# Performance work log

Measured on AMD Instinct MI355X. Metric: run time of the kernel, lower is better.

Reference implementation:

```python
import jax, jax.numpy as jnp
import numpy as np

IN_FEATURES = 4096
OUT_FEATURES = 11008
BLOCK_SIZE = 64

NF4_TABLE = jnp.array([-1.0, -0.6961928009986877, -0.5250730514526367, -0.39491748809814453,
                       -0.28444138169288635, -0.18477343022823334, -0.09105003625154495, 0.0,
                       0.07958029955625534, 0.16093020141124725, 0.24611230194568634,
                       0.33791524171829224, 0.44070982933044434, 0.5626170039176941,
                       0.7229568362236023, 1.0], dtype=jnp.float32)


def setup_inputs() -> dict:
    key = jax.random.key(0)
    k1, k2, k3, k4 = jax.random.split(key, 4)
    n = IN_FEATURES * OUT_FEATURES
    x = jax.random.normal(k1, (4, 128, IN_FEATURES), dtype=jnp.float32)
    # packed 4-bit codes: two codes per byte, flat layout as produced by quantize_and_pack_nf4
    packed_kernel = jax.random.randint(k2, (n // 2,), 0, 256, dtype=jnp.int32).astype(jnp.uint8)
    # per-block absmax scales (positive)
    scales = jax.random.uniform(k3, (n // BLOCK_SIZE,), minval=0.01, maxval=0.05, dtype=jnp.float32)
    bias = jax.random.normal(k4, (OUT_FEATURES,), dtype=jnp.float32) * 0.01
    return {"x": x, "packed_kernel": packed_kernel, "scales": scales, "bias": bias}


def _dequantize_nf4(packed, absmax, block_size):
    high = (packed >> 4) & 15
    low = packed & 15
    # interleave: [h0, l0, h1, l1, ...] matching jnp.stack([high, low], axis=1).reshape(-1)
    unpacked = jnp.stack([high, low], axis=1).reshape(-1)
    deq = NF4_TABLE[unpacked]                       # [n] fp32
    deq = deq.reshape(-1, block_size) * absmax[:, None]  # per-block scaling
    return deq


def reference(x, packed_kernel, scales, bias):
    kernel = _dequantize_nf4(packed_kernel, scales, BLOCK_SIZE).reshape(IN_FEATURES, OUT_FEATURES)
    y = jnp.einsum("bsi,io->bso", x, kernel)
    y = y + bias
    return y
```

## Files before the change

kernel.cpp:

```cpp
#include <hip/hip_runtime.h>
#include <hip/hip_bf16.h>
#include <hip/hip_fp16.h>
#include <stdint.h>

#define K_DIM 4096
#define N_DIM 11008
#define M_DIM 512
#define PK_ROW 5504
#define SC_ROW 172

typedef __attribute__((ext_vector_type(4))) float f32x4;
typedef __attribute__((ext_vector_type(4))) int i32x4;
typedef __attribute__((ext_vector_type(4))) unsigned int u32x4;
typedef __attribute__((ext_vector_type(8))) _Float16 half8;
typedef __attribute__((ext_vector_type(8))) short bf16x8;

__constant__ float NF4[16] = {
    -1.0f, -0.6961928009986877f, -0.5250730514526367f, -0.39491748809814453f,
    -0.28444138169288635f, -0.18477343022823334f, -0.09105003625154495f, 0.0f,
    0.07958029955625534f, 0.16093020141124725f, 0.24611230194568634f,
    0.33791524171829224f, 0.44070982933044434f, 0.5626170039176941f,
    0.7229568362236023f, 1.0f};

union H8 { u32x4 v; half8 h; };

__device__ __forceinline__ unsigned h2mul(unsigned a, unsigned b) {
  union { __half2 h; unsigned u; } x, y, r;
  x.u = a; y.u = b;
  r.h = x.h * y.h;
  return r.u;
}
__device__ __forceinline__ unsigned hpack(float a, float b) {
  union { __half2 h; unsigned u; } c;
  c.h = __floats2half2_rn(a, b);
  return c.u;
}
__device__ __forceinline__ unsigned f2bf(float v) {
  union { __hip_bfloat16 h; unsigned short u; } cv;
  cv.h = __float2bfloat16(v);
  return (unsigned)cv.u;
}

__global__ __launch_bounds__(256) void prep_all(
    const float* __restrict__ x, const int* __restrict__ packed,
    const float* __restrict__ scales, unsigned* __restrict__ wsa,
    unsigned* __restrict__ codes, unsigned* __restrict__ scalesp) {
  const int bid = blockIdx.x;
  const int t = threadIdx.x;
  if (bid < 5504) {
    const int kt = bid & 63;
    const int nt = bid >> 6;
    __shared__ unsigned char Sb[128 * 36];
    const int npl = t & 63;
    const int kq = t >> 6;
    const int np = nt * 64 + npl;
#pragma unroll
    for (int i = 0; i < 8; ++i) {
      const int kpl = kq + i * 4;
      const int k = kt * 64 + kpl * 2;
      const int w0 = packed[(size_t)k * PK_ROW + np];
      const int w1 = packed[(size_t)(k + 1) * PK_ROW + np];
      Sb[(npl * 2) * 36 + kpl] =
          (unsigned char)((((w0 >> 4) & 15) << 4) | ((w1 >> 4) & 15));
      Sb[(npl * 2 + 1) * 36 + kpl] =
          (unsigned char)(((w0 & 15) << 4) | (w1 & 15));
    }
    __syncthreads();
#pragma unroll
    for (int i = 0; i < 4; ++i) {
      const int lin = t + 256 * i;
      const int n16 = lin & 15;
      const int kp4l = (lin >> 4) & 7;
      const int nb16l = lin >> 7;
      const unsigned v = *(const unsigned*)(Sb + (nb16l * 16 + n16) * 36 + kp4l * 4);
      const size_t D = ((size_t)(nt * 8 + nb16l) * 512 + kt * 8 + kp4l) * 16 + n16;
      codes[D] = v;
    }
  } else if (bid < 6528) {
    const int wid = (bid - 5504) * 4 + (t >> 6);
    const int lane = t & 63;
    const int m16 = wid >> 7, k32 = wid & 127;
    const int m = m16 * 16 + (lane & 15);
    const int k = k32 * 32 + (lane >> 4) * 8;
    const float* src = x + (size_t)m * K_DIM + k;
    f32x4 v0 = *(const f32x4*)src;
    f32x4 v1 = *(const f32x4*)(src + 4);
    u32x4 d;
    d[0] = hpack(v0[0], v0[1]);
    d[1] = hpack(v0[2], v0[3]);
    d[2] = hpack(v1[0], v1[1]);
    d[3] = hpack(v1[2], v1[3]);
    *(u32x4*)(wsa + (size_t)wid * 256 + lane * 4) = d;
  } else {
    const int g = (bid - 6528) * 256 + t;
    if (g < SC_ROW * 2048) {
      const int kp = g / SC_ROW;
      const int nb = g - kp * SC_ROW;
      const float s0 = scales[(size_t)(2 * kp) * SC_ROW + nb];
      const float s1 = scales[(size_t)(2 * kp + 1) * SC_ROW + nb];
      scalesp[(size_t)nb * 2048 + kp] = hpack(s0, s1);
    }
  }
}

__global__ __launch_bounds__(256, 3) void nf4_gemm_ib(
    const unsigned* __restrict__ codes, const unsigned* __restrict__ scalesp,
    const unsigned* __restrict__ wsa, const float* __restrict__ bias,
    float* __restrict__ out) {
  __shared__ unsigned LutR[256 * 16];
  __shared__ __align__(16) float Otile[64][132];

  const int bid = blockIdx.x;
  const int x = bid & 7;
  const int local = bid >> 3;
  const int S = (x < 6) ? x * 11 : 66 + (x - 6) * 10;
  const int cnt = (x < 6) ? 11 : 10;
  if (local >= cnt * 8) return;
  const int n_tile = (S + (local >> 3)) * 128;
  const int m_tile = (local & 7) * 64;

  const int t = threadIdx.x;
  {
    const int c = t & 15;
    const int b0 = t >> 4;
#pragma unroll
    for (int i = 0; i < 16; ++i) {
      const int b = b0 + 16 * i;
      LutR[b * 16 + c] = hpack(NF4[(b >> 4) & 15], NF4[b & 15]);
    }
  }
  __syncthreads();

  const int lane = t & 63;
  const int wid = t >> 6;
  const int kh = wid >> 1;
  const int nh = wid & 1;
  const int l15 = lane & 15;
  const int kslice = lane >> 4;
  const int lb = lane & 15;
  const int m16w = m_tile >> 4;
  const int nf0 = (n_tile >> 4) + nh * 4;
  const int nb64 = (n_tile >> 6) + nh;

  unsigned cb[4];
#pragma unroll
  for (int j = 0; j < 4; ++j) cb[j] = (unsigned)(nf0 + j) * 8192 + lane;
  const unsigned sb = (unsigned)nb64 * 2048 + kslice * 4;
  unsigned ab[4];
#pragma unroll
  for (int fm = 0; fm < 4; ++fm)
    ab[fm] = (unsigned)(m16w + fm) * 32768 + lane * 4;

  f32x4 acc[4][4];
#pragma unroll
  for (int i = 0; i < 4; ++i)
#pragma unroll
    for (int j = 0; j < 4; ++j) acc[i][j] = (f32x4){0.f, 0.f, 0.f, 0.f};

  const int NS = 64;
  const int s_base = kh * NS;

  auto LOAD = [&](int sl, unsigned* c, u32x4& sv, u32x4* A) {
    const unsigned s = (unsigned)(s_base + sl);
#pragma unroll
    for (int j = 0; j < 4; ++j) c[j] = codes[cb[j] + 64u * s];
    sv = *(const u32x4*)(scalesp + sb + 16u * s);
#pragma unroll
    for (int fm = 0; fm < 4; ++fm)
      A[fm] = *(const u32x4*)(wsa + ab[fm] + 256u * s);
  };
  auto STEP = [&](const unsigned* c, const u32x4& sv, const u32x4* A) {
    H8 a[4];
#pragma unroll
    for (int fm = 0; fm < 4; ++fm) a[fm].v = A[fm];
#pragma unroll
    for (int j = 0; j < 4; ++j) {
      const unsigned cw = c[j];
      H8 B;
      B.v[0] = h2mul(LutR[((cw & 255u) << 4) | lb], sv[0]);
      B.v[1] = h2mul(LutR[(((cw >> 8) & 255u) << 4) | lb], sv[1]);
      B.v[2] = h2mul(LutR[(((cw >> 16) & 255u) << 4) | lb], sv[2]);
      B.v[3] = h2mul(LutR[((cw >> 24) << 4) | lb], sv[3]);
#pragma unroll
      for (int fm = 0; fm < 4; ++fm)
        acc[fm][j] = __builtin_amdgcn_mfma_f32_16x16x32_f16(a[fm].h, B.h, acc[fm][j], 0, 0, 0);
    }
  };

  unsigned Xc[4], Yc[4];
  u32x4 Xs, Ys;
  u32x4 XA[4], YA[4];
  LOAD(0, Xc, Xs, XA);
#pragma unroll 1
  for (int s = 0; s < NS; s += 2) {
    LOAD(s + 1, Yc, Ys, YA);
    STEP(Xc, Xs, XA);
    if (s + 2 < NS) LOAD(s + 2, Xc, Xs, XA);
    STEP(Yc, Ys, YA);
  }

  if (kh == 1) {
#pragma unroll
    for (int j = 0; j < 4; ++j)
#pragma unroll
      for (int fm = 0; fm < 4; ++fm)
#pragma unroll
        for (int r = 0; r < 4; ++r)
          Otile[fm * 16 + kslice * 4 + r][nh * 64 + j * 16 + l15] = acc[fm][j][r];
  }
  __syncthreads();
  if (kh == 0) {
#pragma unroll
    for (int j = 0; j < 4; ++j) {
      const float bi = bias[n_tile + nh * 64 + j * 16 + l15];
#pragma unroll
      for (int fm = 0; fm < 4; ++fm)
#pragma unroll
        for (int r = 0; r < 4; ++r) {
          const int row = fm * 16 + kslice * 4 + r;
          const int col = nh * 64 + j * 16 + l15;
          Otile[row][col] += acc[fm][j][r] + bi;
        }
    }
  }
  __syncthreads();
  {
    const int c8 = lane & 31;
    const int r2 = lane >> 5;
#pragma unroll
    for (int it = 0; it < 8; ++it) {
      const int row = it * 8 + wid * 2 + r2;
      const f32x4 v = *(const f32x4*)&Otile[row][c8 * 4];
      *(f32x4*)&out[(size_t)(m_tile + row) * N_DIM + n_tile + c8 * 4] = v;
    }
  }
}

#define FLDS 72
__global__ __launch_bounds__(256) void nf4_gemm_fused(
    const float* __restrict__ x, const int* __restrict__ packed,
    const float* __restrict__ scales, const float* __restrict__ bias,
    float* __restrict__ out) {
  __shared__ unsigned short AldsF[128 * FLDS];
  __shared__ unsigned short BldsF[128 * FLDS];
  __shared__ float2 Lut[256];
  const int t = threadIdx.x;
  const int bid = blockIdx.x;
  const int swz = (bid & 7) * 43 + (bid >> 3);
  const int m_tile = (swz / 86) * 128;
  const int n_tile = (swz % 86) * 128;
  Lut[t] = make_float2(NF4[(t >> 4) & 15], NF4[t & 15]);
  const int lane = t & 63;
  const int wid = t >> 6;
  const int wm = (wid >> 1) * 64;
  const int wn = (wid & 1) * 64;
  const int l15 = lane & 15;
  const int l4 = lane >> 4;
  f32x4 acc[4][4];
#pragma unroll
  for (int i = 0; i < 4; ++i)
#pragma unroll
    for (int j = 0; j < 4; ++j) acc[i][j] = (f32x4){0.f, 0.f, 0.f, 0.f};
  const int mlane = t & 15;
  const int n_sub = mlane * 8;
  const int k_sub = 4 * (((t >> 4) + mlane) & 15);
  const int c4 = t & 15;
  const int r0 = t >> 4;
  for (int k0 = 0; k0 < K_DIM; k0 += 64) {
    __syncthreads();
#pragma unroll
    for (int i = 0; i < 8; ++i) {
      const int row = r0 + 16 * i;
      f32x4 xv = *(const f32x4*)(x + (size_t)(m_tile + row) * K_DIM + k0 + c4 * 4);
      uint2 d;
      d.x = f2bf(xv[0]) | (f2bf(xv[1]) << 16);
      d.y = f2bf(xv[2]) | (f2bf(xv[3]) << 16);
      *(uint2*)(&AldsF[row * FLDS + c4 * 4]) = d;
    }
    {
      const int* pk = packed + (size_t)(k0 + k_sub) * PK_ROW + ((n_tile + n_sub) >> 1);
      i32x4 w[4];
      float s[4];
#pragma unroll
      for (int kk = 0; kk < 4; ++kk) {
        w[kk] = *(const i32x4*)(pk + (size_t)kk * PK_ROW);
        s[kk] = scales[(size_t)(k0 + k_sub + kk) * SC_ROW + ((n_tile + n_sub) >> 6)];
      }
      float v[4][8];
#pragma unroll
      for (int kk = 0; kk < 4; ++kk)
#pragma unroll
        for (int e = 0; e < 4; ++e) {
          const int b = w[kk][e] & 0xFF;
          const float2 p = Lut[b];
          v[kk][2 * e] = p.x * s[kk];
          v[kk][2 * e + 1] = p.y * s[kk];
        }
#pragma unroll
      for (int j = 0; j < 8; ++j) {
        uint2 d;
        d.x = f2bf(v[0][j]) | (f2bf(v[1][j]) << 16);
        d.y = f2bf(v[2][j]) | (f2bf(v[3][j]) << 16);
        *(uint2*)(&BldsF[(n_sub + j) * FLDS + k_sub]) = d;
      }
    }
    __syncthreads();
#pragma unroll
    for (int ks = 0; ks < 2; ++ks) {
      bf16x8 af[4], bfv[4];
#pragma unroll
      for (int fm = 0; fm < 4; ++fm)
        af[fm] = *(const bf16x8*)(&AldsF[(wm + fm * 16 + l15) * FLDS + ks * 32 + l4 * 8]);
#pragma unroll
      for (int fn = 0; fn < 4; ++fn)
        bfv[fn] = *(const bf16x8*)(&BldsF[(wn + fn * 16 + l15) * FLDS + ks * 32 + l4 * 8]);
#pragma unroll
      for (int fm = 0; fm < 4; ++fm)
#pragma unroll
        for (int fn = 0; fn < 4; ++fn)
          acc[fm][fn] = __builtin_amdgcn_mfma_f32_16x16x32_bf16(af[fm], bfv[fn], acc[fm][fn], 0, 0, 0);
    }
  }
#pragma unroll
  for (int fn = 0; fn < 4; ++fn) {
    const float bi = bias[n_tile + wn + fn * 16 + l15];
#pragma unroll
    for (int fm = 0; fm < 4; ++fm)
#pragma unroll
      for (int r = 0; r < 4; ++r) {
        const int gr = m_tile + wm + fm * 16 + l4 * 4 + r;
        out[(size_t)gr * N_DIM + n_tile + wn + fn * 16 + l15] = acc[fm][fn][r] + bi;
      }
  }
}

extern "C" void kernel_launch(void* const* d_in, const int* in_sizes, int n_in,
                              void* d_out, int out_size, void* d_ws, size_t ws_size,
                              hipStream_t stream) {
  const float* x = (const float*)d_in[0];
  const int* packed = (const int*)d_in[1];
  const float* scales = (const float*)d_in[2];
  const float* bias = (const float*)d_in[3];
  float* out = (float*)d_out;

  const size_t A_BYTES = (size_t)M_DIM * K_DIM * 2;
  const size_t C_BYTES = (size_t)688 * 512 * 16 * 4;
  const size_t S_BYTES = (size_t)SC_ROW * 2048 * 4;
  const size_t need = A_BYTES + C_BYTES + S_BYTES;

  if (ws_size >= need) {
    unsigned* wsa = (unsigned*)d_ws;
    unsigned* codes = (unsigned*)((char*)d_ws + A_BYTES);
    unsigned* scalesp = (unsigned*)((char*)d_ws + A_BYTES + C_BYTES);
    prep_all<<<dim3(7904), dim3(256), 0, stream>>>(x, packed, scales, wsa, codes, scalesp);
    nf4_gemm_ib<<<dim3(704), dim3(256), 0, stream>>>(codes, scalesp, wsa, bias, out);
  } else {
    nf4_gemm_fused<<<dim3(344), dim3(256), 0, stream>>>(x, packed, scales, bias, out);
  }
}
```

Baseline: 83.14 us.

## Retile NF4 GEMM to 128x64 blocks with four-way split-K per block

The GEMM block tile changes from 64x128 with a 2-way K split and 2-way N split across waves to 128x64, where all four waves cover the full N tile and split K four ways. Each wave now holds 8x4 MFMA accumulators, so each dequantized B fragment feeds eight MFMAs instead of four, cutting LUT lookups and scale multiplies per FLOP. The cross-wave reduction is done in four passes through a smaller shared tile, with extra barriers. Register pressure doubles, so occupancy drops from 3 to 2 blocks per SIMD set.

```diff
diff --git a/kernel.cpp b/kernel.cpp
--- a/kernel.cpp
+++ b/kernel.cpp
@@ -103,21 +103,21 @@
   }
 }
 
-__global__ __launch_bounds__(256, 3) void nf4_gemm_ib(
+__global__ __launch_bounds__(256, 2) void nf4_gemm_ib8(
     const unsigned* __restrict__ codes, const unsigned* __restrict__ scalesp,
     const unsigned* __restrict__ wsa, const float* __restrict__ bias,
     float* __restrict__ out) {
   __shared__ unsigned LutR[256 * 16];
-  __shared__ __align__(16) float Otile[64][132];
+  __shared__ __align__(16) float Otile[32][68];
 
   const int bid = blockIdx.x;
   const int x = bid & 7;
   const int local = bid >> 3;
-  const int S = (x < 6) ? x * 11 : 66 + (x - 6) * 10;
-  const int cnt = (x < 6) ? 11 : 10;
-  if (local >= cnt * 8) return;
-  const int n_tile = (S + (local >> 3)) * 128;
-  const int m_tile = (local & 7) * 64;
+  const int S = (x < 4) ? x * 22 : 88 + (x - 4) * 21;
+  const int cnt = (x < 4) ? 22 : 21;
+  if (local >= cnt * 4) return;
+  const int n_tile = (S + (local >> 2)) * 64;
+  const int m_tile = (local & 3) * 128;
 
   const int t = threadIdx.x;
   {
@@ -132,32 +132,30 @@
   __syncthreads();
 
   const int lane = t & 63;
-  const int wid = t >> 6;
-  const int kh = wid >> 1;
-  const int nh = wid & 1;
+  const int kh = t >> 6;
   const int l15 = lane & 15;
   const int kslice = lane >> 4;
   const int lb = lane & 15;
   const int m16w = m_tile >> 4;
-  const int nf0 = (n_tile >> 4) + nh * 4;
-  const int nb64 = (n_tile >> 6) + nh;
+  const int nf0 = n_tile >> 4;
+  const int nb64 = n_tile >> 6;
 
   unsigned cb[4];
 #pragma unroll
   for (int j = 0; j < 4; ++j) cb[j] = (unsigned)(nf0 + j) * 8192 + lane;
   const unsigned sb = (unsigned)nb64 * 2048 + kslice * 4;
-  unsigned ab[4];
-#pragma unroll
-  for (int fm = 0; fm < 4; ++fm)
+  unsigned ab[8];
+#pragma unroll
+  for (int fm = 0; fm < 8; ++fm)
     ab[fm] = (unsigned)(m16w + fm) * 32768 + lane * 4;
 
-  f32x4 acc[4][4];
-#pragma unroll
-  for (int i = 0; i < 4; ++i)
+  f32x4 acc[8][4];
+#pragma unroll
+  for (int i = 0; i < 8; ++i)
 #pragma unroll
     for (int j = 0; j < 4; ++j) acc[i][j] = (f32x4){0.f, 0.f, 0.f, 0.f};
 
-  const int NS = 64;
+  const int NS = 32;
   const int s_base = kh * NS;
 
   auto LOAD = [&](int sl, unsigned* c, u32x4& sv, u32x4* A) {
@@ -166,13 +164,10 @@
     for (int j = 0; j < 4; ++j) c[j] = codes[cb[j] + 64u * s];
     sv = *(const u32x4*)(scalesp + sb + 16u * s);
 #pragma unroll
-    for (int fm = 0; fm < 4; ++fm)
+    for (int fm = 0; fm < 8; ++fm)
       A[fm] = *(const u32x4*)(wsa + ab[fm] + 256u * s);
   };
   auto STEP = [&](const unsigned* c, const u32x4& sv, const u32x4* A) {
-    H8 a[4];
-#pragma unroll
-    for (int fm = 0; fm < 4; ++fm) a[fm].v = A[fm];
 #pragma unroll
     for (int j = 0; j < 4; ++j) {
       const unsigned cw = c[j];
@@ -182,14 +177,16 @@
       B.v[2] = h2mul(LutR[(((cw >> 16) & 255u) << 4) | lb], sv[2]);
       B.v[3] = h2mul(LutR[((cw >> 24) << 4) | lb], sv[3]);
 #pragma unroll
-      for (int fm = 0; fm < 4; ++fm)
-        acc[fm][j] = __builtin_amdgcn_mfma_f32_16x16x32_f16(a[fm].h, B.h, acc[fm][j], 0, 0, 0);
+      for (int fm = 0; fm < 8; ++fm) {
+        H8 a; a.v = A[fm];
+        acc[fm][j] = __builtin_amdgcn_mfma_f32_16x16x32_f16(a.h, B.h, acc[fm][j], 0, 0, 0);
+      }
     }
   };
 
   unsigned Xc[4], Yc[4];
   u32x4 Xs, Ys;
-  u32x4 XA[4], YA[4];
+  u32x4 XA[8], YA[8];
   LOAD(0, Xc, Xs, XA);
 #pragma unroll 1
   for (int s = 0; s < NS; s += 2) {
@@ -199,40 +196,62 @@
     STEP(Yc, Ys, YA);
   }
 
-  if (kh == 1) {
-#pragma unroll
-    for (int j = 0; j < 4; ++j)
-#pragma unroll
-      for (int fm = 0; fm < 4; ++fm)
-#pragma unroll
-        for (int r = 0; r < 4; ++r)
-          Otile[fm * 16 + kslice * 4 + r][nh * 64 + j * 16 + l15] = acc[fm][j][r];
-  }
-  __syncthreads();
-  if (kh == 0) {
-#pragma unroll
-    for (int j = 0; j < 4; ++j) {
-      const float bi = bias[n_tile + nh * 64 + j * 16 + l15];
-#pragma unroll
-      for (int fm = 0; fm < 4; ++fm)
-#pragma unroll
-        for (int r = 0; r < 4; ++r) {
-          const int row = fm * 16 + kslice * 4 + r;
-          const int col = nh * 64 + j * 16 + l15;
-          Otile[row][col] += acc[fm][j][r] + bi;
-        }
-    }
-  }
-  __syncthreads();
-  {
-    const int c8 = lane & 31;
-    const int r2 = lane >> 5;
-#pragma unroll
-    for (int it = 0; it < 8; ++it) {
-      const int row = it * 8 + wid * 2 + r2;
-      const f32x4 v = *(const f32x4*)&Otile[row][c8 * 4];
-      *(f32x4*)&out[(size_t)(m_tile + row) * N_DIM + n_tile + c8 * 4] = v;
-    }
+#pragma unroll 1
+  for (int p = 0; p < 4; ++p) {
+    if (kh == 1) {
+#pragma unroll
+      for (int j = 0; j < 4; ++j)
+#pragma unroll
+        for (int f = 0; f < 2; ++f)
+#pragma unroll
+          for (int r = 0; r < 4; ++r)
+            Otile[f * 16 + kslice * 4 + r][j * 16 + l15] = acc[2 * p + f][j][r];
+    }
+    __syncthreads();
+    if (kh == 2) {
+#pragma unroll
+      for (int j = 0; j < 4; ++j)
+#pragma unroll
+        for (int f = 0; f < 2; ++f)
+#pragma unroll
+          for (int r = 0; r < 4; ++r)
+            Otile[f * 16 + kslice * 4 + r][j * 16 + l15] += acc[2 * p + f][j][r];
+    }
+    __syncthreads();
+    if (kh == 3) {
+#pragma unroll
+      for (int j = 0; j < 4; ++j)
+#pragma unroll
+        for (int f = 0; f < 2; ++f)
+#pragma unroll
+          for (int r = 0; r < 4; ++r)
+            Otile[f * 16 + kslice * 4 + r][j * 16 + l15] += acc[2 * p + f][j][r];
+    }
+    __syncthreads();
+    if (kh == 0) {
+#pragma unroll
+      for (int j = 0; j < 4; ++j) {
+        const float bi = bias[n_tile + j * 16 + l15];
+#pragma unroll
+        for (int f = 0; f < 2; ++f)
+#pragma unroll
+          for (int r = 0; r < 4; ++r)
+            Otile[f * 16 + kslice * 4 + r][j * 16 + l15] +=
+                acc[2 * p + f][j][r] + bi;
+      }
+    }
+    __syncthreads();
+    {
+      const int c4v = lane & 15;
+      const int r4 = lane >> 4;
+#pragma unroll
+      for (int it = 0; it < 2; ++it) {
+        const int row = it * 16 + kh * 4 + r4;
+        const f32x4 v = *(const f32x4*)&Otile[row][c4v * 4];
+        *(f32x4*)&out[(size_t)(m_tile + p * 32 + row) * N_DIM + n_tile + c4v * 4] = v;
+      }
+    }
+    __syncthreads();
   }
 }
 
@@ -353,7 +372,7 @@
     unsigned* codes = (unsigned*)((char*)d_ws + A_BYTES);
     unsigned* scalesp = (unsigned*)((char*)d_ws + A_BYTES + C_BYTES);
     prep_all<<<dim3(7904), dim3(256), 0, stream>>>(x, packed, scales, wsa, codes, scalesp);
-    nf4_gemm_ib<<<dim3(704), dim3(256), 0, stream>>>(codes, scalesp, wsa, bias, out);
+    nf4_gemm_ib8<<<dim3(704), dim3(256), 0, stream>>>(codes, scalesp, wsa, bias, out);
   } else {
     nf4_gemm_fused<<<dim3(344), dim3(256), 0, stream>>>(x, packed, scales, bias, out);
   }
```

Result: slower. 116.2 us (+39.7%).
